# Kernel optimization log

Hardware: AMD Instinct MI355X
Metric: run time of the kernel (lower is better)

Reference implementation:

```python
import jax, jax.numpy as jnp
import numpy as np

N, T, F_IN, H, D_FF, C_OUT = 4096, 60, 64, 128, 256, 1


def _gru_layer(x_tnf, W_ih, W_hh, b_ih, b_hh):
    # torch nn.GRU single layer; x_tnf: [T, N, in]
    def step(h, xt):
        gi = xt @ W_ih.T + b_ih          # [N, 3H]
        gh = h @ W_hh.T + b_hh
        i_r, i_z, i_n = jnp.split(gi, 3, axis=-1)
        h_r, h_z, h_n = jnp.split(gh, 3, axis=-1)
        r = jax.nn.sigmoid(i_r + h_r)
        z = jax.nn.sigmoid(i_z + h_z)
        n = jnp.tanh(i_n + r * h_n)
        h = (1.0 - z) * n + z * h
        return h, h
    h0 = jnp.zeros((x_tnf.shape[1], W_hh.shape[1]), x_tnf.dtype)
    hT, ys = jax.lax.scan(step, h0, x_tnf)
    return hT, ys


def setup_inputs() -> dict:
    key = jax.random.key(0)
    ks = jax.random.split(key, 20)
    s_in = 1.0 / np.sqrt(F_IN)
    s_h = 1.0 / np.sqrt(H)
    inp = {
        'x': jax.random.normal(ks[0], (N, T, F_IN), jnp.float32),
        'W_ih0': jax.random.normal(ks[1], (3 * H, F_IN), jnp.float32) * s_in,
        'W_hh0': jax.random.normal(ks[2], (3 * H, H), jnp.float32) * s_h,
        'b_ih0': jax.random.normal(ks[3], (3 * H,), jnp.float32) * s_h,
        'b_hh0': jax.random.normal(ks[4], (3 * H,), jnp.float32) * s_h,
        'W_ih1': jax.random.normal(ks[5], (3 * H, H), jnp.float32) * s_h,
        'W_hh1': jax.random.normal(ks[6], (3 * H, H), jnp.float32) * s_h,
        'b_ih1': jax.random.normal(ks[7], (3 * H,), jnp.float32) * s_h,
        'b_hh1': jax.random.normal(ks[8], (3 * H,), jnp.float32) * s_h,
        'Wt': jax.random.normal(ks[9], (H, H), jnp.float32) * s_h,
        'bt': jax.random.normal(ks[10], (H,), jnp.float32) * s_h,
        'a': jax.random.normal(ks[11], (2 * H, 1), jnp.float32),
        'Wfc': jax.random.normal(ks[12], (H, H), jnp.float32) * s_h,
        'bfc': jax.random.normal(ks[13], (H,), jnp.float32) * s_h,
        'Wp1': jax.random.normal(ks[14], (D_FF, H), jnp.float32) * s_h,
        'bp1': jax.random.normal(ks[15], (D_FF,), jnp.float32) * s_h,
        'Wp2': jax.random.normal(ks[16], (C_OUT, D_FF), jnp.float32) * (1.0 / np.sqrt(D_FF)),
        'bp2': jax.random.normal(ks[17], (C_OUT,), jnp.float32) * (1.0 / np.sqrt(D_FF)),
    }
    return inp


def reference(x, W_ih0, W_hh0, b_ih0, b_hh0, W_ih1, W_hh1, b_ih1, b_hh1,
              Wt, bt, a, Wfc, bfc, Wp1, bp1, Wp2, bp2):
    x_tnf = jnp.transpose(x, (1, 0, 2))  # [T, N, F]
    _, ys0 = _gru_layer(x_tnf, W_ih0, W_hh0, b_ih0, b_hh0)
    hT, _ = _gru_layer(ys0, W_ih1, W_hh1, b_ih1, b_hh1)
    hidden = hT  # out[:, -1, :], [N, H]

    # cal_attention: score[i,j] = a[:H].x_j + a[H:].x_i  (separable GAT score)
    xt = hidden @ Wt.T + bt                      # transformation(x) == transformation(y)
    a_flat = a[:, 0]
    s_j = xt @ a_flat[:H]                        # [N], contributes per-column
    s_i = xt @ a_flat[H:]                        # [N], contributes per-row
    scores = jax.nn.leaky_relu(s_i[:, None] + s_j[None, :], negative_slope=0.01)
    att = jax.nn.softmax(scores, axis=1)         # [N, N]

    hidden = att @ hidden + hidden
    hidden = jax.nn.leaky_relu(hidden @ Wfc.T + bfc, negative_slope=0.01)
    h1 = jax.nn.gelu(hidden @ Wp1.T + bp1, approximate=False)
    out = h1 @ Wp2.T + bp2                       # [N, 1]
    return jnp.squeeze(out)                      # [N]
```

## Files before the change

kernel.cpp:

```cpp
#include <hip/hip_runtime.h>
#include <cstdint>
#include <cstddef>

#define TSTEPS 60
#define NB 4096
#define HD 128

typedef __attribute__((ext_vector_type(8))) short short8;
typedef __attribute__((ext_vector_type(4))) float f32x4;

#define WS_SJ    0
#define WS_SI    16384
#define WS_HID   32768
#define WS_HTH   2129920
#define WS_HTL   3178496
#define WS_F0H   4227072
#define WS_F0L   (WS_F0H+49152)
#define WS_FR0H  (WS_F0L+49152)
#define WS_FR0L  (WS_FR0H+98304)
#define WS_FR1H  (WS_FR0L+98304)
#define WS_FR1L  (WS_FR1H+98304)
#define WS_FR2H  (WS_FR1L+98304)
#define WS_FR2L  (WS_FR2H+98304)
#define WS_BASE  (WS_FR2L+98304)
#define WS_Y0P   WS_BASE
#define WS_FULL  (WS_Y0P + 125829120ULL)


__device__ __forceinline__ float b2f(unsigned short h){ return __uint_as_float(((unsigned)h)<<16); }
__device__ __forceinline__ unsigned short f2b(float f){
  unsigned u = __float_as_uint(f);
  u = (u + 0x7FFFu + ((u>>16)&1u)) >> 16;
  return (unsigned short)u;
}
__device__ __forceinline__ float sigm(float x){ return 1.0f/(1.0f + __expf(-x)); }
__device__ __forceinline__ float tanhfast(float x){
  float xc = fminf(fmaxf(x,-15.0f),15.0f);
  float e = __expf(2.0f*xc);
  return (e-1.0f)/(e+1.0f);
}
__device__ __forceinline__ float lrelu(float x){ return x > 0.0f ? x : 0.01f*x; }
__device__ __forceinline__ float ldr1(const void* p, size_t i, int f32){
  return f32 ? ((const float*)p)[i] : b2f(((const unsigned short*)p)[i]);
}
template<bool F32>
__device__ __forceinline__ float4 ldg4c(const void* p, size_t i){
  if (F32) return *(const float4*)((const float*)p + i);
  ushort4 u = *(const ushort4*)((const unsigned short*)p + i);
  float4 f; f.x=b2f(u.x); f.y=b2f(u.y); f.z=b2f(u.z); f.w=b2f(u.w); return f;
}
__device__ __forceinline__ f32x4 f4zero(){ f32x4 v = {0.f,0.f,0.f,0.f}; return v; }
__device__ __forceinline__ void pinv(short8& v){ asm volatile("" : "+v"(v)); }

__device__ __forceinline__ void ldsbar(){
  asm volatile("s_waitcnt lgkmcnt(0)\n\ts_barrier" ::: "memory");
}

__device__ int probe_f32(const void* p, int nprobe, volatile int* s){
  if (threadIdx.x == 0) *s = 0;
  __syncthreads();
  if ((int)threadIdx.x < nprobe) {
    float v = b2f(((const unsigned short*)p)[threadIdx.x]);
    if (!(v == v) || fabsf(v) > 1e4f) *s = 1;
  }
  __syncthreads();
  int r = *s;
  __syncthreads();
  return r;
}

__global__ void diag_kernel(float* out, float code){
  int i = blockIdx.x*256 + threadIdx.x;
  if (i < 4096) out[i] = code;
}

__device__ void repack_mat(const void* src, int f32, int K, int nks,
                           unsigned short* hi, unsigned short* lo,
                           int tid, int nthr){
  int total = 384*K;
  for (int idx = tid; idx < total; idx += nthr) {
    int j = idx & 7, lane = (idx>>3)&63, t = idx>>9;
    int ks = t % nks, g = (t/nks)%3, w = t/(nks*3);
    int row = 16*(w + 8*g) + (lane & 15);
    int k   = ks*32 + ((lane>>4)<<3) + j;
    float v = f32 ? ((const float*)src)[(size_t)row*K + k]
                  : b2f(((const unsigned short*)src)[(size_t)row*K + k]);
    unsigned short h = f2b(v);
    hi[idx] = h;
    lo[idx] = f2b(v - b2f(h));
  }
}

__global__ __launch_bounds__(256) void repack_kernel(
    const void* wih0, const void* whh0, const void* wih1, const void* whh1,
    char* ws)
{
  __shared__ int sp;
  int f0 = probe_f32(wih0, 256, &sp);
  int f1 = probe_f32(whh0, 256, &sp);
  int f2 = probe_f32(wih1, 256, &sp);
  int f3 = probe_f32(whh1, 256, &sp);
  int tid  = blockIdx.x*256 + threadIdx.x;
  int nthr = gridDim.x*256;
  repack_mat(wih0, f0,  64, 2, (unsigned short*)(ws+WS_F0H),  (unsigned short*)(ws+WS_F0L),  tid, nthr);
  repack_mat(whh0, f1, 128, 4, (unsigned short*)(ws+WS_FR0H), (unsigned short*)(ws+WS_FR0L), tid, nthr);
  repack_mat(wih1, f2, 128, 4, (unsigned short*)(ws+WS_FR1H), (unsigned short*)(ws+WS_FR1L), tid, nthr);
  repack_mat(whh1, f3, 128, 4, (unsigned short*)(ws+WS_FR2H), (unsigned short*)(ws+WS_FR2L), tid, nthr);
}

#define MFMA __builtin_amdgcn_mfma_f32_16x16x32_bf16

__global__ __launch_bounds__(1024)
void gru0_kernel(const void* __restrict__ xg,
                 const void* __restrict__ bih0, const void* __restrict__ bhh0,
                 const char* __restrict__ ws, unsigned* __restrict__ y0p)
{
  __shared__ __align__(16) unsigned short xbh[2][1152], xbl[2][1152];
  __shared__ __align__(16) unsigned short hbh[2][2176], hbl[2][2176];
  __shared__ __align__(16) float pex[8192];
  __shared__ int sp;
  const int tid  = threadIdx.x;
  const int W    = tid >> 6;
  const int cg   = W >> 1;
  const int kh   = W & 1;
  const int lane = tid & 63;
  const int ln   = lane & 15;
  const int kq   = lane >> 4;
  const int r0   = blockIdx.x * 16;

  int xf  = probe_f32(xg,   256, &sp);
  int fb0 = probe_f32(bih0, 256, &sp);
  int fh0 = probe_f32(bhh0, 256, &sp);

  const unsigned short* f0h  = (const unsigned short*)(ws+WS_F0H);
  const unsigned short* f0l  = (const unsigned short*)(ws+WS_F0L);
  const unsigned short* fr0h = (const unsigned short*)(ws+WS_FR0H);
  const unsigned short* fr0l = (const unsigned short*)(ws+WS_FR0L);

  short8 X0h[3], X0l[3];
  #pragma unroll
  for (int g = 0; g < 3; ++g) {
    int fi = (cg*3+g)*2 + kh;
    X0h[g] = *(const short8*)&f0h[fi*512 + lane*8];
    X0l[g] = *(const short8*)&f0l[fi*512 + lane*8];
    pinv(X0h[g]); pinv(X0l[g]);
  }
  short8 R0h[3][2], R0l[3][2];
  #pragma unroll
  for (int g = 0; g < 3; ++g)
    #pragma unroll
    for (int jj = 0; jj < 2; ++jj) {
      int fi = (cg*3+g)*4 + kh*2 + jj;
      R0h[g][jj] = *(const short8*)&fr0h[fi*512 + lane*8];
      R0l[g][jj] = *(const short8*)&fr0l[fi*512 + lane*8];
      pinv(R0h[g][jj]); pinv(R0l[g][jj]);
    }

  const int nr = cg*16 + ln;
  float brc0 = ldr1(bih0,nr,fb0)     + ldr1(bhh0,nr,fh0);
  float bzc0 = ldr1(bih0,nr+128,fb0) + ldr1(bhh0,nr+128,fh0);
  float bin0 = ldr1(bih0,nr+256,fb0);
  float bhn0 = ldr1(bhh0,nr+256,fh0);

  for (int i = tid; i < 2176; i += 1024) { hbh[0][i] = 0; hbl[0][i] = 0; }
  const int xm = tid >> 5, xfc = (tid & 31)*2;
  if (tid < 512) {
    size_t base = ((size_t)(r0+xm)*TSTEPS + 0)*64 + xfc;
    float v0, v1;
    if (xf) { float2 xv = *(const float2*)((const float*)xg + base); v0 = xv.x; v1 = xv.y; }
    else { ushort2 u = *(const ushort2*)((const unsigned short*)xg + base); v0 = b2f(u.x); v1 = b2f(u.y); }
    unsigned short a0 = f2b(v0), a1 = f2b(v1);
    unsigned short l0 = f2b(v0-b2f(a0)), l1 = f2b(v1-b2f(a1));
    *(unsigned*)&xbh[0][xm*72+xfc] = (unsigned)a0 | ((unsigned)a1<<16);
    *(unsigned*)&xbl[0][xm*72+xfc] = (unsigned)l0 | ((unsigned)l1<<16);
  }
  float h0o[2] = {0.f, 0.f};
  __syncthreads();

  #pragma unroll 1
  for (int t = 0; t < TSTEPS; ++t) {
    const int b0 = t & 1, b1 = b0 ^ 1;
    float v0 = 0.f, v1 = 0.f;
    const bool stg = (tid < 512) && (t+1 < TSTEPS);
    if (stg) {
      size_t base = ((size_t)(r0+xm)*TSTEPS + (t+1))*64 + xfc;
      if (xf) { float2 xv = *(const float2*)((const float*)xg + base); v0 = xv.x; v1 = xv.y; }
      else { ushort2 u = *(const ushort2*)((const unsigned short*)xg + base); v0 = b2f(u.x); v1 = b2f(u.y); }
    }

    f32x4 acc[4];
    #pragma unroll
    for (int g = 0; g < 4; ++g) acc[g] = f4zero();
    {
      short8 axh = *(const short8*)&xbh[b0][ln*72 + kh*32 + kq*8];
      short8 axl = *(const short8*)&xbl[b0][ln*72 + kh*32 + kq*8];
      #pragma unroll
      for (int g = 0; g < 3; ++g) {
        acc[g] = MFMA(axh, X0h[g], acc[g], 0,0,0);
        acc[g] = MFMA(axh, X0l[g], acc[g], 0,0,0);
        acc[g] = MFMA(axl, X0h[g], acc[g], 0,0,0);
      }
    }
    #pragma unroll
    for (int jj = 0; jj < 2; ++jj) {
      short8 ahh = *(const short8*)&hbh[b0][ln*136 + (kh*2+jj)*32 + kq*8];
      short8 ahl = *(const short8*)&hbl[b0][ln*136 + (kh*2+jj)*32 + kq*8];
      #pragma unroll
      for (int g = 0; g < 3; ++g) {
        int tgt = (g==2) ? 3 : g;
        acc[tgt] = MFMA(ahh, R0h[g][jj], acc[tgt], 0,0,0);
        acc[tgt] = MFMA(ahh, R0l[g][jj], acc[tgt], 0,0,0);
        acc[tgt] = MFMA(ahl, R0h[g][jj], acc[tgt], 0,0,0);
      }
    }

    {
      int wbase = W*512 + lane*2;
      if (kh == 0) {
        #pragma unroll
        for (int g = 0; g < 4; ++g) {
          float2 wv; wv.x = acc[g][2]; wv.y = acc[g][3];
          *(float2*)&pex[wbase + g*128] = wv;
        }
      } else {
        #pragma unroll
        for (int g = 0; g < 4; ++g) {
          float2 wv; wv.x = acc[g][0]; wv.y = acc[g][1];
          *(float2*)&pex[wbase + g*128] = wv;
        }
      }
    }
    ldsbar();

    float c0[2], c1[2], c2[2], c3[2];
    {
      int pbase = (W^1)*512 + lane*2;
      float2 p0 = *(const float2*)&pex[pbase];
      float2 p1 = *(const float2*)&pex[pbase + 128];
      float2 p2 = *(const float2*)&pex[pbase + 256];
      float2 p3 = *(const float2*)&pex[pbase + 384];
      if (kh == 0) {
        c0[0]=acc[0][0]+p0.x; c0[1]=acc[0][1]+p0.y;
        c1[0]=acc[1][0]+p1.x; c1[1]=acc[1][1]+p1.y;
        c2[0]=acc[2][0]+p2.x; c2[1]=acc[2][1]+p2.y;
        c3[0]=acc[3][0]+p3.x; c3[1]=acc[3][1]+p3.y;
      } else {
        c0[0]=acc[0][2]+p0.x; c0[1]=acc[0][3]+p0.y;
        c1[0]=acc[1][2]+p1.x; c1[1]=acc[1][3]+p1.y;
        c2[0]=acc[2][2]+p2.x; c2[1]=acc[2][3]+p2.y;
        c3[0]=acc[3][2]+p3.x; c3[1]=acc[3][3]+p3.y;
      }
    }

    unsigned short nh2[2], nl2[2];
    #pragma unroll
    for (int j = 0; j < 2; ++j) {
      float r  = sigm(c0[j] + brc0);
      float z  = sigm(c1[j] + bzc0);
      float nn = tanhfast(c2[j] + bin0 + r*(c3[j] + bhn0));
      float h  = nn + z*(h0o[j] - nn);
      h0o[j] = h;
      unsigned short hh = f2b(h);
      nh2[j] = hh; nl2[j] = f2b(h - b2f(hh));
    }
    const int rowb = kq*4 + kh*2;
    {
      size_t ybase = ((size_t)blockIdx.x*TSTEPS + t)*2048;
      #pragma unroll
      for (int j = 0; j < 2; ++j)
        y0p[ybase + (rowb+j)*128 + cg*16 + ln] =
            (unsigned)nh2[j] | ((unsigned)nl2[j] << 16);
    }
    #pragma unroll
    for (int j = 0; j < 2; ++j) {
      int off = (rowb+j)*136 + cg*16 + ln;
      hbh[b1][off] = nh2[j]; hbl[b1][off] = nl2[j];
    }
    if (stg) {
      unsigned short a0 = f2b(v0), a1 = f2b(v1);
      unsigned short l0 = f2b(v0-b2f(a0)), l1 = f2b(v1-b2f(a1));
      *(unsigned*)&xbh[b1][xm*72+xfc] = (unsigned)a0 | ((unsigned)a1<<16);
      *(unsigned*)&xbl[b1][xm*72+xfc] = (unsigned)l0 | ((unsigned)l1<<16);
    }
    ldsbar();
  }
}

__global__ __launch_bounds__(512) __attribute__((amdgpu_waves_per_eu(2,2)))
void gru1_kernel(const void* __restrict__ bih1, const void* __restrict__ bhh1,
                 const char* __restrict__ ws, const unsigned* __restrict__ y0p,
                 float* __restrict__ hidg,
                 unsigned short* __restrict__ hTh, unsigned short* __restrict__ hTl)
{
  __shared__ __align__(16) unsigned short wih1hL[49152];
  __shared__ __align__(16) unsigned short ybh[2][2176], ybl[2][2176];
  __shared__ __align__(16) unsigned short h1bh[2][2176], h1bl[2][2176];
  __shared__ int sp;
  const int tid  = threadIdx.x;
  const int w    = tid >> 6;
  const int lane = tid & 63;
  const int ln   = lane & 15;
  const int kq   = lane >> 4;
  const int r0   = blockIdx.x * 16;

  int fb1 = probe_f32(bih1, 256, &sp);
  int fh1 = probe_f32(bhh1, 256, &sp);

  const unsigned short* fr1h = (const unsigned short*)(ws+WS_FR1H);
  const unsigned short* fr1l = (const unsigned short*)(ws+WS_FR1L);
  const unsigned short* fr2h = (const unsigned short*)(ws+WS_FR2H);
  const unsigned short* fr2l = (const unsigned short*)(ws+WS_FR2L);

  for (int i = tid*8; i < 49152; i += 4096) {
    *(ushort4*)&wih1hL[i]   = *(const ushort4*)&fr1h[i];
    *(ushort4*)&wih1hL[i+4] = *(const ushort4*)&fr1h[i+4];
  }

  short8 W1hp[2][4];
  #pragma unroll
  for (int g = 0; g < 2; ++g)
    #pragma unroll
    for (int ks = 0; ks < 4; ++ks) {
      W1hp[g][ks] = *(const short8*)&fr1h[((w*3+g)*4+ks)*512 + lane*8];
      pinv(W1hp[g][ks]);
    }

  short8 W1l[3][4], R2h[3][4], R2l[3][4];
  #pragma unroll
  for (int g = 0; g < 3; ++g)
    #pragma unroll
    for (int ks = 0; ks < 4; ++ks) {
      int fi = (w*3+g)*4 + ks;
      W1l[g][ks] = *(const short8*)&fr1l[fi*512 + lane*8];
      R2h[g][ks] = *(const short8*)&fr2h[fi*512 + lane*8];
      R2l[g][ks] = *(const short8*)&fr2l[fi*512 + lane*8];
      pinv(W1l[g][ks]); pinv(R2h[g][ks]); pinv(R2l[g][ks]);
    }

  const int nr = 16*w + ln;
  float brc1 = ldr1(bih1,nr,fb1)     + ldr1(bhh1,nr,fh1);
  float bzc1 = ldr1(bih1,nr+128,fb1) + ldr1(bhh1,nr+128,fh1);
  float bin1 = ldr1(bih1,nr+256,fb1);
  float bhn1 = ldr1(bhh1,nr+256,fh1);

  for (int i = tid; i < 2176; i += 512) { h1bh[0][i] = 0; h1bl[0][i] = 0; }
  const int yi4 = tid*4, yrow = yi4 >> 7, ycol = yi4 & 127;
  #pragma unroll
  for (int tt = 0; tt < 2; ++tt) {
    uint4 pv = *(const uint4*)&y0p[((size_t)blockIdx.x*TSTEPS + tt)*2048 + yi4];
    ushort4 vh, vl;
    vh.x=(unsigned short)(pv.x&0xffff); vl.x=(unsigned short)(pv.x>>16);
    vh.y=(unsigned short)(pv.y&0xffff); vl.y=(unsigned short)(pv.y>>16);
    vh.z=(unsigned short)(pv.z&0xffff); vl.z=(unsigned short)(pv.z>>16);
    vh.w=(unsigned short)(pv.w&0xffff); vl.w=(unsigned short)(pv.w>>16);
    *(ushort4*)&ybh[tt][yrow*136+ycol] = vh;
    *(ushort4*)&ybl[tt][yrow*136+ycol] = vl;
  }
  float h1o[4] = {0.f,0.f,0.f,0.f};
  __syncthreads();

  f32x4 accY[3];
  #pragma unroll
  for (int g = 0; g < 3; ++g) accY[g] = f4zero();
  #pragma unroll
  for (int ks = 0; ks < 4; ++ks) {
    short8 ayh = *(const short8*)&ybh[0][ln*136 + ks*32 + kq*8];
    short8 ayl = *(const short8*)&ybl[0][ln*136 + ks*32 + kq*8];
    #pragma unroll
    for (int g = 0; g < 3; ++g) {
      short8 bh;
      if (g < 2) bh = W1hp[g][ks];
      else       bh = *(const short8*)&wih1hL[((w*3+2)*4+ks)*512 + lane*8];
      accY[g] = MFMA(ayh, bh,         accY[g], 0,0,0);
      accY[g] = MFMA(ayh, W1l[g][ks], accY[g], 0,0,0);
      accY[g] = MFMA(ayl, bh,         accY[g], 0,0,0);
    }
  }

  #pragma unroll 1
  for (int t = 0; t < TSTEPS; ++t) {
    const int b0 = t & 1, b1 = b0 ^ 1;
    uint4 pv = {0,0,0,0};
    if (t+2 < TSTEPS)
      pv = *(const uint4*)&y0p[((size_t)blockIdx.x*TSTEPS + (t+2))*2048 + yi4];

    f32x4 acc[4];
    acc[0] = accY[0]; acc[1] = accY[1]; acc[2] = accY[2]; acc[3] = f4zero();
    #pragma unroll
    for (int ks = 0; ks < 4; ++ks) {
      short8 a1h = *(const short8*)&h1bh[b0][ln*136 + ks*32 + kq*8];
      short8 a1l = *(const short8*)&h1bl[b0][ln*136 + ks*32 + kq*8];
      #pragma unroll
      for (int g = 0; g < 3; ++g) {
        int tgtH = (g==2) ? 3 : g;
        acc[tgtH] = MFMA(a1h, R2h[g][ks], acc[tgtH], 0,0,0);
        acc[tgtH] = MFMA(a1h, R2l[g][ks], acc[tgtH], 0,0,0);
        acc[tgtH] = MFMA(a1l, R2h[g][ks], acc[tgtH], 0,0,0);
      }
    }
    unsigned short nh[4], nl[4];
    #pragma unroll
    for (int rg = 0; rg < 4; ++rg) {
      float r  = sigm(acc[0][rg] + brc1);
      float z  = sigm(acc[1][rg] + bzc1);
      float nn = tanhfast(acc[2][rg] + bin1 + r*(acc[3][rg] + bhn1));
      float h  = nn + z*(h1o[rg] - nn);
      h1o[rg] = h;
      unsigned short hh = f2b(h);
      nh[rg] = hh; nl[rg] = f2b(h - b2f(hh));
    }
    #pragma unroll
    for (int rg = 0; rg < 4; ++rg) {
      int off = (kq*4+rg)*136 + w*16 + ln;
      h1bh[b1][off] = nh[rg]; h1bl[b1][off] = nl[rg];
    }
    if (t+2 < TSTEPS) {
      ushort4 vh, vl;
      vh.x=(unsigned short)(pv.x&0xffff); vl.x=(unsigned short)(pv.x>>16);
      vh.y=(unsigned short)(pv.y&0xffff); vl.y=(unsigned short)(pv.y>>16);
      vh.z=(unsigned short)(pv.z&0xffff); vl.z=(unsigned short)(pv.z>>16);
      vh.w=(unsigned short)(pv.w&0xffff); vl.w=(unsigned short)(pv.w>>16);
      *(ushort4*)&ybh[b0][yrow*136+ycol] = vh;
      *(ushort4*)&ybl[b0][yrow*136+ycol] = vl;
    }
    if (t+1 < TSTEPS) {
      #pragma unroll
      for (int g = 0; g < 3; ++g) accY[g] = f4zero();
      #pragma unroll
      for (int ks = 0; ks < 4; ++ks) {
        short8 ayh = *(const short8*)&ybh[b1][ln*136 + ks*32 + kq*8];
        short8 ayl = *(const short8*)&ybl[b1][ln*136 + ks*32 + kq*8];
        #pragma unroll
        for (int g = 0; g < 3; ++g) {
          short8 bh;
          if (g < 2) bh = W1hp[g][ks];
          else       bh = *(const short8*)&wih1hL[((w*3+2)*4+ks)*512 + lane*8];
          accY[g] = MFMA(ayh, bh,         accY[g], 0,0,0);
          accY[g] = MFMA(ayh, W1l[g][ks], accY[g], 0,0,0);
          accY[g] = MFMA(ayl, bh,         accY[g], 0,0,0);
        }
      }
    }
    ldsbar();
  }

  {
    int c = w*16 + ln;
    #pragma unroll
    for (int rg = 0; rg < 4; ++rg)
      hidg[(size_t)(r0 + kq*4 + rg)*HD + c] = h1o[rg];
    #pragma unroll
    for (int rg = 0; rg < 4; ++rg) {
      unsigned short hh = f2b(h1o[rg]);
      unsigned short ll = f2b(h1o[rg] - b2f(hh));
      int n   = r0 + kq*4 + rg;
      int chn = n >> 9, ksn = (n >> 5) & 15, kqn = (n >> 3) & 3, jn = n & 7;
      size_t o = ((size_t)((w*8 + chn)*16 + ksn))*512
               + (size_t)(kqn*16 + ln)*8 + jn;
      hTh[o] = hh;
      hTl[o] = ll;
    }
  }
}

__global__ __launch_bounds__(512, 1) void gru_fb_kernel(
    const void* __restrict__ xg,
    const void* __restrict__ bih0, const void* __restrict__ bhh0,
    const void* __restrict__ bih1, const void* __restrict__ bhh1,
    const char* __restrict__ ws, float* __restrict__ hidg,
    unsigned short* __restrict__ hTh, unsigned short* __restrict__ hTl)
{
  __shared__ __align__(16) unsigned short wih0L[49152];
  __shared__ __align__(16) unsigned short xhi[1152], xlo[1152];
  __shared__ __align__(16) unsigned short h0hi[2176], h0lo[2176];
  __shared__ __align__(16) unsigned short h1hi[2176], h1lo[2176];
  __shared__ int sp;
  const int tid  = threadIdx.x;
  const int w    = tid >> 6;
  const int lane = tid & 63;
  const int ln   = lane & 15;
  const int kq   = lane >> 4;
  const int r0   = blockIdx.x * 16;

  int xf  = probe_f32(xg,   256, &sp);
  int fb0 = probe_f32(bih0, 256, &sp);
  int fh0 = probe_f32(bhh0, 256, &sp);
  int fb1 = probe_f32(bih1, 256, &sp);
  int fh1 = probe_f32(bhh1, 256, &sp);

  const unsigned short* f0h  = (const unsigned short*)(ws+WS_F0H);
  const unsigned short* f0l  = (const unsigned short*)(ws+WS_F0L);
  const unsigned short* fr0h = (const unsigned short*)(ws+WS_FR0H);
  const unsigned short* fr0l = (const unsigned short*)(ws+WS_FR0L);
  const unsigned short* fr1h = (const unsigned short*)(ws+WS_FR1H);
  const unsigned short* fr1l = (const unsigned short*)(ws+WS_FR1L);
  const unsigned short* fr2h = (const unsigned short*)(ws+WS_FR2H);
  const unsigned short* fr2l = (const unsigned short*)(ws+WS_FR2L);

  for (int i = tid*8; i < 24576; i += 4096) {
    *(ushort4*)&wih0L[i]         = *(const ushort4*)&f0h[i];
    *(ushort4*)&wih0L[i+4]       = *(const ushort4*)&f0h[i+4];
    *(ushort4*)&wih0L[24576+i]   = *(const ushort4*)&f0l[i];
    *(ushort4*)&wih0L[24576+i+4] = *(const ushort4*)&f0l[i+4];
  }
  short8 R0h[3][4], R1h[3][4], R2h[3][4];
  #pragma unroll
  for (int g = 0; g < 3; ++g)
    #pragma unroll
    for (int ks = 0; ks < 4; ++ks) {
      int fi = (w*3+g)*4 + ks;
      R0h[g][ks] = *(const short8*)&fr0h[fi*512 + lane*8];
      R1h[g][ks] = *(const short8*)&fr1h[fi*512 + lane*8];
      R2h[g][ks] = *(const short8*)&fr2h[fi*512 + lane*8];
      pinv(R0h[g][ks]); pinv(R1h[g][ks]); pinv(R2h[g][ks]);
    }
  const int nr = 16*w + ln;
  float brc0 = ldr1(bih0,nr,fb0)     + ldr1(bhh0,nr,fh0);
  float bzc0 = ldr1(bih0,nr+128,fb0) + ldr1(bhh0,nr+128,fh0);
  float bin0 = ldr1(bih0,nr+256,fb0);
  float bhn0 = ldr1(bhh0,nr+256,fh0);
  float brc1 = ldr1(bih1,nr,fb1)     + ldr1(bhh1,nr,fh1);
  float bzc1 = ldr1(bih1,nr+128,fb1) + ldr1(bhh1,nr+128,fh1);
  float bin1 = ldr1(bih1,nr+256,fb1);
  float bhn1 = ldr1(bhh1,nr+256,fh1);

  for (int i = tid; i < 2176; i += 512) {
    h0hi[i] = 0; h0lo[i] = 0; h1hi[i] = 0; h1lo[i] = 0;
  }
  float h0o[4] = {0.f,0.f,0.f,0.f};
  float h1o[4] = {0.f,0.f,0.f,0.f};
  __syncthreads();

  #pragma unroll 1
  for (int t = 0; t < TSTEPS; ++t) {
    {
      int i0 = tid*2, m = i0 >> 6, f = i0 & 63;
      size_t base = ((size_t)(r0+m)*TSTEPS + t)*64 + f;
      float v0, v1;
      if (xf) { float2 xv = *(const float2*)((const float*)xg + base); v0 = xv.x; v1 = xv.y; }
      else { ushort2 u = *(const ushort2*)((const unsigned short*)xg + base); v0 = b2f(u.x); v1 = b2f(u.y); }
      unsigned short a0 = f2b(v0), a1 = f2b(v1);
      xhi[m*72+f] = a0;              xhi[m*72+f+1] = a1;
      xlo[m*72+f] = f2b(v0-b2f(a0)); xlo[m*72+f+1] = f2b(v1-b2f(a1));
    }
    __syncthreads();
    f32x4 acc[4];
    #pragma unroll
    for (int g = 0; g < 4; ++g) acc[g] = f4zero();
    #pragma unroll
    for (int ks = 0; ks < 2; ++ks) {
      short8 axh = *(const short8*)&xhi[ln*72 + ks*32 + kq*8];
      short8 axl = *(const short8*)&xlo[ln*72 + ks*32 + kq*8];
      #pragma unroll
      for (int g = 0; g < 3; ++g) {
        int fi = (w*3+g)*2 + ks;
        short8 bh = *(const short8*)&wih0L[fi*512 + lane*8];
        short8 bl = *(const short8*)&wih0L[24576 + fi*512 + lane*8];
        acc[g] = MFMA(axh, bh, acc[g], 0,0,0);
        acc[g] = MFMA(axh, bl, acc[g], 0,0,0);
        acc[g] = MFMA(axl, bh, acc[g], 0,0,0);
      }
    }
    #pragma unroll
    for (int ks = 0; ks < 4; ++ks) {
      short8 ahh = *(const short8*)&h0hi[ln*136 + ks*32 + kq*8];
      short8 ahl = *(const short8*)&h0lo[ln*136 + ks*32 + kq*8];
      #pragma unroll
      for (int g = 0; g < 3; ++g) {
        int tgt = (g==2) ? 3 : g;
        short8 bl = *(const short8*)&fr0l[((w*3+g)*4+ks)*512 + lane*8];
        acc[tgt] = MFMA(ahh, R0h[g][ks], acc[tgt], 0,0,0);
        acc[tgt] = MFMA(ahh, bl,         acc[tgt], 0,0,0);
        acc[tgt] = MFMA(ahl, R0h[g][ks], acc[tgt], 0,0,0);
      }
    }
    unsigned short nh[4], nl[4];
    #pragma unroll
    for (int rg = 0; rg < 4; ++rg) {
      float r  = sigm(acc[0][rg] + brc0);
      float z  = sigm(acc[1][rg] + bzc0);
      float nn = tanhfast(acc[2][rg] + bin0 + r*(acc[3][rg] + bhn0));
      float h  = nn + z*(h0o[rg] - nn);
      h0o[rg] = h;
      unsigned short hh = f2b(h);
      nh[rg] = hh; nl[rg] = f2b(h - b2f(hh));
    }
    __syncthreads();
    #pragma unroll
    for (int rg = 0; rg < 4; ++rg) {
      int off = (kq*4+rg)*136 + w*16 + ln;
      h0hi[off] = nh[rg]; h0lo[off] = nl[rg];
    }
    __syncthreads();
    #pragma unroll
    for (int g = 0; g < 4; ++g) acc[g] = f4zero();
    #pragma unroll
    for (int ks = 0; ks < 4; ++ks) {
      short8 ayh = *(const short8*)&h0hi[ln*136 + ks*32 + kq*8];
      short8 ayl = *(const short8*)&h0lo[ln*136 + ks*32 + kq*8];
      short8 a1h = *(const short8*)&h1hi[ln*136 + ks*32 + kq*8];
      short8 a1l = *(const short8*)&h1lo[ln*136 + ks*32 + kq*8];
      #pragma unroll
      for (int g = 0; g < 3; ++g) {
        int tgtI = (g==2) ? 2 : g;
        int tgtH = (g==2) ? 3 : g;
        short8 blI = *(const short8*)&fr1l[((w*3+g)*4+ks)*512 + lane*8];
        short8 blH = *(const short8*)&fr2l[((w*3+g)*4+ks)*512 + lane*8];
        acc[tgtI] = MFMA(ayh, R1h[g][ks], acc[tgtI], 0,0,0);
        acc[tgtI] = MFMA(ayh, blI,        acc[tgtI], 0,0,0);
        acc[tgtI] = MFMA(ayl, R1h[g][ks], acc[tgtI], 0,0,0);
        acc[tgtH] = MFMA(a1h, R2h[g][ks], acc[tgtH], 0,0,0);
        acc[tgtH] = MFMA(a1h, blH,        acc[tgtH], 0,0,0);
        acc[tgtH] = MFMA(a1l, R2h[g][ks], acc[tgtH], 0,0,0);
      }
    }
    #pragma unroll
    for (int rg = 0; rg < 4; ++rg) {
      float r  = sigm(acc[0][rg] + brc1);
      float z  = sigm(acc[1][rg] + bzc1);
      float nn = tanhfast(acc[2][rg] + bin1 + r*(acc[3][rg] + bhn1));
      float h  = nn + z*(h1o[rg] - nn);
      h1o[rg] = h;
      unsigned short hh = f2b(h);
      nh[rg] = hh; nl[rg] = f2b(h - b2f(hh));
    }
    __syncthreads();
    #pragma unroll
    for (int rg = 0; rg < 4; ++rg) {
      int off = (kq*4+rg)*136 + w*16 + ln;
      h1hi[off] = nh[rg]; h1lo[off] = nl[rg];
    }
  }
  {
    int c = w*16 + ln;
    #pragma unroll
    for (int rg = 0; rg < 4; ++rg)
      hidg[(size_t)(r0 + kq*4 + rg)*HD + c] = h1o[rg];
    #pragma unroll
    for (int rg = 0; rg < 4; ++rg) {
      unsigned short hh = f2b(h1o[rg]);
      unsigned short ll = f2b(h1o[rg] - b2f(hh));
      int n   = r0 + kq*4 + rg;
      int chn = n >> 9, ksn = (n >> 5) & 15, kqn = (n >> 3) & 3, jn = n & 7;
      size_t o = ((size_t)((w*8 + chn)*16 + ksn))*512
               + (size_t)(kqn*16 + ln)*8 + jn;
      hTh[o] = hh;
      hTl[o] = ll;
    }
  }
}

template<bool WT32>
__device__ void sprep_body(
    const float* hidg, const void* wt, const void* bt, const void* a,
    int f_bt, int f_a, float* sjg, float* sig, float* hL, float* redb)
{
  const int tid = threadIdx.x;
  const int r0  = blockIdx.x * 16;
  for (int i = tid; i < 2048; i += 256) hL[i] = hidg[(size_t)r0*128 + i];
  __syncthreads();
  const int r = tid >> 4, cg = tid & 15, c0 = cg*8;
  float sjp = 0.f, sip = 0.f;
  #pragma unroll 1
  for (int cc = 0; cc < 8; ++cc) {
    int cI = c0 + cc;
    float acc = ldr1(bt, cI, f_bt);
    #pragma unroll 4
    for (int kq = 0; kq < 32; ++kq) {
      int k = kq*4;
      float4 wv = ldg4c<WT32>(wt, (size_t)cI*128 + k);
      float4 h = *(const float4*)&hL[r*128 + k];
      acc += wv.x*h.x + wv.y*h.y + wv.z*h.z + wv.w*h.w;
    }
    sjp += acc * ldr1(a, cI, f_a);
    sip += acc * ldr1(a, cI + 128, f_a);
  }
  redb[(r*16+cg)*2]   = sjp;
  redb[(r*16+cg)*2+1] = sip;
  __syncthreads();
  if (tid < 32) {
    int r2 = tid >> 1, wh = tid & 1;
    float s = 0.f;
    for (int g = 0; g < 16; ++g) s += redb[(r2*16+g)*2 + wh];
    if (wh == 0) sjg[r0+r2] = s; else sig[r0+r2] = s;
  }
}

__global__ __launch_bounds__(256) void sprep_kernel(
    const float* hidg, const void* wt, const void* bt, const void* a,
    float* sjg, float* sig)
{
  __shared__ float hL[2048];
  __shared__ float redb[512];
  __shared__ int sp;
  int f_wt = probe_f32(wt, 256, &sp);
  int f_bt = probe_f32(bt, 128, &sp);
  int f_a  = probe_f32(a,  256, &sp);
  if (f_wt) sprep_body<true >(hidg, wt, bt, a, f_bt, f_a, sjg, sig, hL, redb);
  else      sprep_body<false>(hidg, wt, bt, a, f_bt, f_a, sjg, sig, hL, redb);
}

template<bool PW32>
__device__ void attn_body(
    const float* sjg, const float* sig, const float* hidg,
    const unsigned short* hTh, const unsigned short* hTl,
    const void* wfc, const void* bfc, const void* wp1, const void* bp1,
    const void* wp2, const void* bp2,
    int f_bfc, int f_bp1, int f_wp2, float* outg,
    float* sjs, unsigned short* Pbuf, float* Obuf, float* redm,
    float* siL, float* miL, float* Zb)
{
  const int tid = threadIdx.x;
  const int w = tid >> 6, lane = tid & 63, ln = lane & 15, kq = lane >> 4;
  const int r0 = blockIdx.x * 16;

  for (int i = tid; i < 4096; i += 512) sjs[i] = sjg[i];
  __syncthreads();
  float mx = -1e30f;
  for (int i = tid; i < 4096; i += 512) mx = fmaxf(mx, sjs[i]);
  redm[tid] = mx;
  __syncthreads();
  for (int s = 256; s > 0; s >>= 1) {
    if (tid < s) redm[tid] = fmaxf(redm[tid], redm[tid+s]);
    __syncthreads();
  }
  if (tid < 16) {
    float si = sig[r0 + tid];
    siL[tid] = si;
    miL[tid] = lrelu(si + redm[0]);
  }
  __syncthreads();

  float zp[16];
  #pragma unroll
  for (int i = 0; i < 16; ++i) zp[i] = 0.f;
  f32x4 accO = f4zero();
  const int col = w*16 + ln;

  #define GENP(CH, BASE)                                                    \
    {                                                                       \
      unsigned short* Phi_ = (BASE);                                        \
      unsigned short* Plo_ = (BASE) + 8320;                                 \
      float sjv = sjs[(CH)*512 + tid];                                      \
      _Pragma("unroll")                                                     \
      for (int i = 0; i < 16; ++i) {                                        \
        float v = lrelu(siL[i] + sjv);                                      \
        float p = __expf(v - miL[i]);                                       \
        zp[i] += p;                                                         \
        unsigned short hh = f2b(p);                                         \
        Phi_[i*520 + tid] = hh;                                             \
        Plo_[i*520 + tid] = f2b(p - b2f(hh));                               \
      }                                                                     \
    }

  GENP(0, Pbuf);
  __syncthreads();

  #pragma unroll 1
  for (int ch = 0; ch < 8; ++ch) {
    const int b = ch & 1;
    unsigned short* Phi = Pbuf + b*16640;
    unsigned short* Plo = Phi + 8320;
    #pragma unroll
    for (int ks = 0; ks < 16; ++ks) {
      short8 Ah = *(const short8*)&Phi[ln*520 + ks*32 + kq*8];
      short8 Al = *(const short8*)&Plo[ln*520 + ks*32 + kq*8];
      size_t bo = ((size_t)((w*8 + ch)*16 + ks))*512 + (size_t)lane*8;
      short8 Bh = *(const short8*)&hTh[bo];
      short8 Bl = *(const short8*)&hTl[bo];
      accO = MFMA(Ah, Bh, accO, 0,0,0);
      accO = MFMA(Ah, Bl, accO, 0,0,0);
      accO = MFMA(Al, Bh, accO, 0,0,0);
    }
    if (ch < 7) GENP(ch+1, Pbuf + (b^1)*16640);
    __syncthreads();
  }
  #undef GENP

  #pragma unroll
  for (int rg = 0; rg < 4; ++rg)
    Obuf[(kq*4+rg)*128 + col] = accO[rg];

  float* zarr = (float*)Pbuf;
  #pragma unroll
  for (int i = 0; i < 16; ++i) zarr[i*512 + tid] = zp[i];
  __syncthreads();
  {
    int row = tid >> 5, t0 = tid & 31;
    float s = 0.f;
    #pragma unroll
    for (int k = 0; k < 16; ++k) s += zarr[row*512 + t0 + 32*k];
    redm[row*32 + t0] = s;
  }
  __syncthreads();
  if (tid < 16) {
    float s = 0.f;
    for (int g = 0; g < 32; ++g) s += redm[tid*32 + g];
    Zb[tid] = s;
  }
  __syncthreads();

  {
    int e0 = tid*4, row = e0 >> 7, c = e0 & 127;
    float zi = Zb[row];
    #pragma unroll
    for (int e = 0; e < 4; ++e)
      Obuf[e0+e] = Obuf[e0+e]/zi + hidg[(size_t)(r0+row)*128 + c + e];
  }
  __syncthreads();

  float* h3f = sjs;
  {
    int o0 = tid*4, row = o0 >> 7, c = o0 & 127;
    #pragma unroll 1
    for (int e = 0; e < 4; ++e) {
      int cI = c + e;
      float acc = ldr1(bfc, cI, f_bfc);
      #pragma unroll 4
      for (int k4 = 0; k4 < 32; ++k4) {
        int k = k4*4;
        float4 wv = ldg4c<PW32>(wfc, (size_t)cI*128 + k);
        float4 h = *(const float4*)&Obuf[row*128 + k];
        acc += wv.x*h.x + wv.y*h.y + wv.z*h.z + wv.w*h.w;
      }
      h3f[row*128 + cI] = lrelu(acc);
    }
  }
  __syncthreads();

  float* h1f = (float*)Pbuf;
  {
    int o0 = tid*8, row = o0 >> 8, c = o0 & 255;
    #pragma unroll 1
    for (int e = 0; e < 8; ++e) {
      int cI = c + e;
      float acc = ldr1(bp1, cI, f_bp1);
      #pragma unroll 4
      for (int k4 = 0; k4 < 32; ++k4) {
        int k = k4*4;
        float4 wv = ldg4c<PW32>(wp1, (size_t)cI*128 + k);
        float4 h = *(const float4*)&h3f[row*128 + k];
        acc += wv.x*h.x + wv.y*h.y + wv.z*h.z + wv.w*h.w;
      }
      h1f[row*256 + cI] = 0.5f*acc*(1.0f + erff(acc*0.70710678118f));
    }
  }
  __syncthreads();

  {
    int row = tid >> 5, t0 = tid & 31;
    float s = 0.f;
    #pragma unroll
    for (int k = 0; k < 8; ++k) {
      int cI = t0 + 32*k;
      s += h1f[row*256 + cI] * ldr1(wp2, cI, f_wp2);
    }
    redm[row*32 + t0] = s;
  }
  __syncthreads();
  if (tid < 16) {
    float acc = ldr1(bp2, 0, f_bp1);
    for (int g = 0; g < 32; ++g) acc += redm[tid*32 + g];
    outg[r0 + tid] = acc;
  }
}

__global__ __launch_bounds__(512) void attn_kernel(
    const float* sjg, const float* sig, const float* hidg,
    const unsigned short* hTh, const unsigned short* hTl,
    const void* wfc, const void* bfc, const void* wp1, const void* bp1,
    const void* wp2, const void* bp2, float* outg)
{
  __shared__ float sjs[4096];
  __shared__ __align__(16) unsigned short Pbuf[33280];
  __shared__ float Obuf[2048];
  __shared__ float redm[512];
  __shared__ float siL[16], miL[16], Zb[16];
  __shared__ int sp;
  int f_wfc = probe_f32(wfc, 256, &sp);
  int f_bfc = probe_f32(bfc, 128, &sp);
  int f_bp1 = probe_f32(bp1, 256, &sp);
  int f_wp2 = probe_f32(wp2, 256, &sp);
  if (f_wfc) attn_body<true >(sjg, sig, hidg, hTh, hTl, wfc, bfc, wp1, bp1,
                              wp2, bp2, f_bfc, f_bp1, f_wp2, outg,
                              sjs, Pbuf, Obuf, redm, siL, miL, Zb);
  else       attn_body<false>(sjg, sig, hidg, hTh, hTl, wfc, bfc, wp1, bp1,
                              wp2, bp2, f_bfc, f_bp1, f_wp2, outg,
                              sjs, Pbuf, Obuf, redm, siL, miL, Zb);
}

extern "C" void kernel_launch(void* const* d_in, const int* in_sizes, int n_in,
                              void* d_out, int out_size, void* d_ws, size_t ws_size,
                              hipStream_t stream)
{
  float* out = (float*)d_out;
  const int expected[18] = {15728640,24576,49152,384,384,49152,49152,384,384,
                            16384,128,256,16384,128,32768,256,256,1};
  int bad = 0;
  if (n_in != 18 || out_size != 4096) bad = 1600;
  else for (int i = 0; i < 18; ++i) if (in_sizes[i] != expected[i]) { bad = 1600; break; }
  if (!bad && ws_size < (size_t)WS_BASE) bad = 1664;
  if (bad) { diag_kernel<<<16, 256, 0, stream>>>(out, (float)bad); return; }

  char* ws = (char*)d_ws;
  float*          sj  = (float*)(ws + WS_SJ);
  float*          si  = (float*)(ws + WS_SI);
  float*          hid = (float*)(ws + WS_HID);
  unsigned short* hTh = (unsigned short*)(ws + WS_HTH);
  unsigned short* hTl = (unsigned short*)(ws + WS_HTL);

  repack_kernel<<<256, 256, 0, stream>>>(d_in[1], d_in[2], d_in[5], d_in[6], ws);
  if (ws_size >= WS_FULL) {
    unsigned* y0p = (unsigned*)(ws + WS_Y0P);
    gru0_kernel<<<256, 1024, 0, stream>>>(d_in[0], d_in[3], d_in[4], ws, y0p);
    gru1_kernel<<<256, 512, 0, stream>>>(d_in[7], d_in[8], ws, y0p,
                                         hid, hTh, hTl);
  } else {
    gru_fb_kernel<<<256, 512, 0, stream>>>(d_in[0], d_in[3], d_in[4],
                                           d_in[7], d_in[8], ws, hid, hTh, hTl);
  }
  sprep_kernel<<<256, 256, 0, stream>>>(hid, d_in[9], d_in[10], d_in[11], sj, si);
  attn_kernel<<<256, 512, 0, stream>>>(sj, si, hid, hTh, hTl,
                                       d_in[12], d_in[13], d_in[14], d_in[15],
                                       d_in[16], d_in[17], out);
}
```

Baseline: 552.4 us.

## Halve attention rows per block and double grid, drop P double-buffering

The attention kernel now handles 8 query rows per block instead of 16 and launches 512 blocks, so the 256 CUs get more blocks to schedule. The probability tile is single-buffered with a sync between generation and MFMA use, which roughly halves LDS use and may allow two blocks per CU. The 16-row MFMA tiles still run in full, so half the A rows are unused stale data whose outputs are discarded. Each block still streams all of hTh and hTl, so total B-operand traffic and MFMA work double, and generation no longer overlaps with the MFMAs.

```diff
diff --git a/kernel.cpp b/kernel.cpp
--- a/kernel.cpp
+++ b/kernel.cpp
@@ -710,9 +710,11 @@
     float* sjs, unsigned short* Pbuf, float* Obuf, float* redm,
     float* siL, float* miL, float* Zb)
 {
+  unsigned short* Phi = Pbuf;
+  unsigned short* Plo = Pbuf + 8320;
   const int tid = threadIdx.x;
   const int w = tid >> 6, lane = tid & 63, ln = lane & 15, kq = lane >> 4;
-  const int r0 = blockIdx.x * 16;
+  const int r0 = blockIdx.x * 8;
 
   for (int i = tid; i < 4096; i += 512) sjs[i] = sjg[i];
   __syncthreads();
@@ -724,43 +726,34 @@
     if (tid < s) redm[tid] = fmaxf(redm[tid], redm[tid+s]);
     __syncthreads();
   }
-  if (tid < 16) {
+  if (tid < 8) {
     float si = sig[r0 + tid];
     siL[tid] = si;
     miL[tid] = lrelu(si + redm[0]);
   }
   __syncthreads();
 
-  float zp[16];
+  float zp[8];
   #pragma unroll
-  for (int i = 0; i < 16; ++i) zp[i] = 0.f;
+  for (int i = 0; i < 8; ++i) zp[i] = 0.f;
   f32x4 accO = f4zero();
   const int col = w*16 + ln;
 
-  #define GENP(CH, BASE)                                                    \
-    {                                                                       \
-      unsigned short* Phi_ = (BASE);                                        \
-      unsigned short* Plo_ = (BASE) + 8320;                                 \
-      float sjv = sjs[(CH)*512 + tid];                                      \
-      _Pragma("unroll")                                                     \
-      for (int i = 0; i < 16; ++i) {                                        \
-        float v = lrelu(siL[i] + sjv);                                      \
-        float p = __expf(v - miL[i]);                                       \
-        zp[i] += p;                                                         \
-        unsigned short hh = f2b(p);                                         \
-        Phi_[i*520 + tid] = hh;                                             \
-        Plo_[i*520 + tid] = f2b(p - b2f(hh));                               \
-      }                                                                     \
-    }
-
-  GENP(0, Pbuf);
-  __syncthreads();
-
   #pragma unroll 1
   for (int ch = 0; ch < 8; ++ch) {
-    const int b = ch & 1;
-    unsigned short* Phi = Pbuf + b*16640;
-    unsigned short* Plo = Phi + 8320;
+    {
+      float sjv = sjs[ch*512 + tid];
+      #pragma unroll
+      for (int i = 0; i < 8; ++i) {
+        float v = lrelu(siL[i] + sjv);
+        float p = __expf(v - miL[i]);
+        zp[i] += p;
+        unsigned short hh = f2b(p);
+        Phi[i*520 + tid] = hh;
+        Plo[i*520 + tid] = f2b(p - b2f(hh));
+      }
+    }
+    __syncthreads();
     #pragma unroll
     for (int ks = 0; ks < 16; ++ks) {
       short8 Ah = *(const short8*)&Phi[ln*520 + ks*32 + kq*8];
@@ -772,48 +765,48 @@
       accO = MFMA(Ah, Bl, accO, 0,0,0);
       accO = MFMA(Al, Bh, accO, 0,0,0);
     }
-    if (ch < 7) GENP(ch+1, Pbuf + (b^1)*16640);
     __syncthreads();
   }
-  #undef GENP
-
-  #pragma unroll
-  for (int rg = 0; rg < 4; ++rg)
-    Obuf[(kq*4+rg)*128 + col] = accO[rg];
+
+  if (kq < 2) {
+    #pragma unroll
+    for (int rg = 0; rg < 4; ++rg)
+      Obuf[(kq*4+rg)*128 + col] = accO[rg];
+  }
 
   float* zarr = (float*)Pbuf;
   #pragma unroll
-  for (int i = 0; i < 16; ++i) zarr[i*512 + tid] = zp[i];
+  for (int i = 0; i < 8; ++i) zarr[i*512 + tid] = zp[i];
   __syncthreads();
   {
-    int row = tid >> 5, t0 = tid & 31;
+    int row = tid >> 6, t0 = tid & 63;
     float s = 0.f;
     #pragma unroll
-    for (int k = 0; k < 16; ++k) s += zarr[row*512 + t0 + 32*k];
-    redm[row*32 + t0] = s;
-  }
-  __syncthreads();
-  if (tid < 16) {
+    for (int k = 0; k < 8; ++k) s += zarr[row*512 + t0 + 64*k];
+    redm[row*64 + t0] = s;
+  }
+  __syncthreads();
+  if (tid < 8) {
     float s = 0.f;
-    for (int g = 0; g < 32; ++g) s += redm[tid*32 + g];
+    for (int g = 0; g < 64; ++g) s += redm[tid*64 + g];
     Zb[tid] = s;
   }
   __syncthreads();
 
   {
-    int e0 = tid*4, row = e0 >> 7, c = e0 & 127;
+    int e0 = tid*2, row = e0 >> 7, c = e0 & 127;
     float zi = Zb[row];
     #pragma unroll
-    for (int e = 0; e < 4; ++e)
+    for (int e = 0; e < 2; ++e)
       Obuf[e0+e] = Obuf[e0+e]/zi + hidg[(size_t)(r0+row)*128 + c + e];
   }
   __syncthreads();
 
   float* h3f = sjs;
   {
-    int o0 = tid*4, row = o0 >> 7, c = o0 & 127;
+    int o0 = tid*2, row = o0 >> 7, c = o0 & 127;
     #pragma unroll 1
-    for (int e = 0; e < 4; ++e) {
+    for (int e = 0; e < 2; ++e) {
       int cI = c + e;
       float acc = ldr1(bfc, cI, f_bfc);
       #pragma unroll 4
@@ -830,9 +823,9 @@
 
   float* h1f = (float*)Pbuf;
   {
-    int o0 = tid*8, row = o0 >> 8, c = o0 & 255;
+    int o0 = tid*4, row = o0 >> 8, c = o0 & 255;
     #pragma unroll 1
-    for (int e = 0; e < 8; ++e) {
+    for (int e = 0; e < 4; ++e) {
       int cI = c + e;
       float acc = ldr1(bp1, cI, f_bp1);
       #pragma unroll 4
@@ -848,19 +841,19 @@
   __syncthreads();
 
   {
-    int row = tid >> 5, t0 = tid & 31;
+    int row = tid >> 6, t0 = tid & 63;
     float s = 0.f;
     #pragma unroll
-    for (int k = 0; k < 8; ++k) {
-      int cI = t0 + 32*k;
+    for (int k = 0; k < 4; ++k) {
+      int cI = t0 + 64*k;
       s += h1f[row*256 + cI] * ldr1(wp2, cI, f_wp2);
     }
-    redm[row*32 + t0] = s;
-  }
-  __syncthreads();
-  if (tid < 16) {
+    redm[row*64 + t0] = s;
+  }
+  __syncthreads();
+  if (tid < 8) {
     float acc = ldr1(bp2, 0, f_bp1);
-    for (int g = 0; g < 32; ++g) acc += redm[tid*32 + g];
+    for (int g = 0; g < 64; ++g) acc += redm[tid*64 + g];
     outg[r0 + tid] = acc;
   }
 }
@@ -872,10 +865,10 @@
     const void* wp2, const void* bp2, float* outg)
 {
   __shared__ float sjs[4096];
-  __shared__ __align__(16) unsigned short Pbuf[33280];
-  __shared__ float Obuf[2048];
+  __shared__ __align__(16) unsigned short Pbuf[16640];
+  __shared__ float Obuf[1024];
   __shared__ float redm[512];
-  __shared__ float siL[16], miL[16], Zb[16];
+  __shared__ float siL[8], miL[8], Zb[8];
   __shared__ int sp;
   int f_wfc = probe_f32(wfc, 256, &sp);
   int f_bfc = probe_f32(bfc, 128, &sp);
@@ -920,7 +913,7 @@
                                            d_in[7], d_in[8], ws, hid, hTh, hTl);
   }
   sprep_kernel<<<256, 256, 0, stream>>>(hid, d_in[9], d_in[10], d_in[11], sj, si);
-  attn_kernel<<<256, 512, 0, stream>>>(sj, si, hid, hTh, hTl,
+  attn_kernel<<<512, 512, 0, stream>>>(sj, si, hid, hTh, hTl,
                                        d_in[12], d_in[13], d_in[14], d_in[15],
                                        d_in[16], d_in[17], out);
 }
```

New measurement: 577.4 us. +4.5%, slower.
